# Kernel tuning notes

Hardware: AMD Instinct MI355X
Metric: run time of the kernel (lower is better)

Reference implementation:

```python
import jax, jax.numpy as jnp
import numpy as np

D_MODEL = 1024
NUM_HEADS = 16
D_K = D_MODEL // NUM_HEADS


def setup_inputs() -> dict:
    key = jax.random.key(0)
    ks = jax.random.split(key, 11)
    B, S = 2, 2048
    scale = 1.0 / np.sqrt(D_MODEL)
    inp = {
        "Q": jax.random.normal(ks[0], (B, S, D_MODEL), jnp.float32),
        "K": jax.random.normal(ks[1], (B, S, D_MODEL), jnp.float32),
        "V": jax.random.normal(ks[2], (B, S, D_MODEL), jnp.float32),
        # per-head projection weights stacked on head axis: [H, d_model, d_k]
        "Wq": jax.random.uniform(ks[3], (NUM_HEADS, D_MODEL, D_K), jnp.float32, -scale, scale),
        "bq": jax.random.uniform(ks[4], (NUM_HEADS, D_K), jnp.float32, -scale, scale),
        "Wk": jax.random.uniform(ks[5], (NUM_HEADS, D_MODEL, D_K), jnp.float32, -scale, scale),
        "bk": jax.random.uniform(ks[6], (NUM_HEADS, D_K), jnp.float32, -scale, scale),
        "Wv": jax.random.uniform(ks[7], (NUM_HEADS, D_MODEL, D_K), jnp.float32, -scale, scale),
        "bv": jax.random.uniform(ks[8], (NUM_HEADS, D_K), jnp.float32, -scale, scale),
        "Wo": jax.random.uniform(ks[9], (D_MODEL, D_MODEL), jnp.float32, -scale, scale),
        "bo": jax.random.uniform(ks[10], (D_MODEL,), jnp.float32, -scale, scale),
    }
    return inp


def reference(Q, K, V, Wq, bq, Wk, bk, Wv, bv, Wo, bo):
    # Batched equivalent of the per-head loop: project all heads at once.
    q = jnp.einsum("bsd,hdk->bhsk", Q, Wq) + bq[None, :, None, :]
    k = jnp.einsum("bsd,hdk->bhsk", K, Wk) + bk[None, :, None, :]
    v = jnp.einsum("bsd,hdk->bhsk", V, Wv) + bv[None, :, None, :]
    scores = jnp.einsum("bhqk,bhmk->bhqm", q, k) / jnp.sqrt(jnp.float32(D_K))
    weights = jax.nn.softmax(scores, axis=-1)
    attn = jnp.einsum("bhqm,bhmk->bhqk", weights, v)  # [B,H,S,d_k]
    B, H, S, Dk = attn.shape
    concat = attn.transpose(0, 2, 1, 3).reshape(B, S, H * Dk)  # head-order concat
    return concat @ Wo.T + bo
```

## Files before the change

kernel.cpp:

```cpp
#include <hip/hip_runtime.h>
#include <math.h>

#define BATCH 2
#define SLEN 2048
#define DM 1024
#define NH 16
#define DK 64
#define STILES (SLEN / 64)

typedef __attribute__((ext_vector_type(8))) __bf16 bf16x8;
typedef __attribute__((ext_vector_type(4))) float f32x4;

__device__ __forceinline__ unsigned short f2bf(float x) {
  unsigned u = __builtin_bit_cast(unsigned, x);
  unsigned r = (u + 0x7fffu + ((u >> 16) & 1u)) >> 16;
  return (unsigned short)r;
}
__device__ __forceinline__ void splitbf(float x, unsigned short& h,
                                        unsigned short& l) {
  unsigned u = __builtin_bit_cast(unsigned, x);
  h = (unsigned short)(u >> 16);
  float hf = __builtin_bit_cast(float, u & 0xffff0000u);
  l = (unsigned short)(__builtin_bit_cast(unsigned, x - hf) >> 16);
}

__device__ __forceinline__ void gld16(const unsigned short* g,
                                      unsigned short* l) {
  __builtin_amdgcn_global_load_lds(
      (const __attribute__((address_space(1))) void*)g,
      (__attribute__((address_space(3))) void*)l, 16, 0, 0);
}

__global__ __launch_bounds__(256)
void convert_w(const float* __restrict__ Wq, const float* __restrict__ Wk,
               const float* __restrict__ Wv, unsigned short* __restrict__ Wqt,
               unsigned short* __restrict__ Wkt,
               unsigned short* __restrict__ Wvt) {
  const int kb = blockIdx.x, h = blockIdx.y, z = blockIdx.z;
  const float* W = (z == 0 ? Wq : z == 1 ? Wk : Wv) +
                   ((size_t)h * DM + kb * 64) * DK;
  unsigned short* D = (z == 0 ? Wqt : z == 1 ? Wkt : Wvt);

  __shared__ float T[64][65];
  const int tid = threadIdx.x;
  {
    int r = tid >> 2, c0 = (tid & 3) * 16;
#pragma unroll
    for (int i = 0; i < 4; ++i) {
      float4 f = *(const float4*)(W + (size_t)r * DK + c0 + i * 4);
      T[r][c0 + i * 4 + 0] = f.x;
      T[r][c0 + i * 4 + 1] = f.y;
      T[r][c0 + i * 4 + 2] = f.z;
      T[r][c0 + i * 4 + 3] = f.w;
    }
  }
  __syncthreads();
  int j = tid >> 2, p = tid & 3;
  int n = h * 64 + j;
  int kloc = p * 16;
  unsigned short hi[16], lo[16];
#pragma unroll
  for (int i = 0; i < 16; ++i) splitbf(T[kloc + i][j], hi[i], lo[i]);
  int kglob = kb * 64 + kloc;
  int blk = kglob >> 5;
  int c0 = (kglob & 31) >> 3;
  int key = n & 7;
  unsigned short* rowp = D + (size_t)n * 2048 + blk * 64;
  uint4 u0, u1;
  u0.x = (unsigned)hi[0] | ((unsigned)hi[1] << 16);
  u0.y = (unsigned)hi[2] | ((unsigned)hi[3] << 16);
  u0.z = (unsigned)hi[4] | ((unsigned)hi[5] << 16);
  u0.w = (unsigned)hi[6] | ((unsigned)hi[7] << 16);
  u1.x = (unsigned)hi[8] | ((unsigned)hi[9] << 16);
  u1.y = (unsigned)hi[10] | ((unsigned)hi[11] << 16);
  u1.z = (unsigned)hi[12] | ((unsigned)hi[13] << 16);
  u1.w = (unsigned)hi[14] | ((unsigned)hi[15] << 16);
  *(uint4*)(rowp + ((c0 ^ key)) * 8) = u0;
  *(uint4*)(rowp + (((c0 + 1) ^ key)) * 8) = u1;
  u0.x = (unsigned)lo[0] | ((unsigned)lo[1] << 16);
  u0.y = (unsigned)lo[2] | ((unsigned)lo[3] << 16);
  u0.z = (unsigned)lo[4] | ((unsigned)lo[5] << 16);
  u0.w = (unsigned)lo[6] | ((unsigned)lo[7] << 16);
  u1.x = (unsigned)lo[8] | ((unsigned)lo[9] << 16);
  u1.y = (unsigned)lo[10] | ((unsigned)lo[11] << 16);
  u1.z = (unsigned)lo[12] | ((unsigned)lo[13] << 16);
  u1.w = (unsigned)lo[14] | ((unsigned)lo[15] << 16);
  *(uint4*)(rowp + (((c0 + 4) ^ key)) * 8) = u0;
  *(uint4*)(rowp + (((c0 + 5) ^ key)) * 8) = u1;
}

__global__ __launch_bounds__(256)
void convert_x(const float* __restrict__ Q, const float* __restrict__ K,
               const float* __restrict__ V, unsigned short* __restrict__ Xp) {
  const int m = blockIdx.x, z = blockIdx.y;
  const float* src = (z == 0 ? Q : z == 1 ? K : V) + (size_t)m * DM;
  unsigned short* dst =
      Xp + (size_t)z * (8u * 1024 * 1024) + (size_t)m * 2048;
  const int k0 = threadIdx.x * 4;
  float4 f = *(const float4*)(src + k0);
  ushort4 h4, l4;
  splitbf(f.x, h4.x, l4.x);
  splitbf(f.y, h4.y, l4.y);
  splitbf(f.z, h4.z, l4.z);
  splitbf(f.w, h4.w, l4.w);
  int blk = k0 >> 5, ch = (k0 & 31) >> 3, off = k0 & 7, key = m & 7;
  unsigned short* rowp = dst + blk * 64;
  *(ushort4*)(rowp + ((ch ^ key)) * 8 + off) = h4;
  *(ushort4*)(rowp + (((ch + 4) ^ key)) * 8 + off) = l4;
}

__global__ __launch_bounds__(256)
void convert_wo(const float* __restrict__ Wo, unsigned short* __restrict__ Wot) {
  const int n = blockIdx.x;
  const int t = threadIdx.x;
  const int k0 = t * 4;
  float4 f = *(const float4*)(Wo + (size_t)n * DM + k0);
  ushort4 h4, l4;
  splitbf(f.x, h4.x, l4.x);
  splitbf(f.y, h4.y, l4.y);
  splitbf(f.z, h4.z, l4.z);
  splitbf(f.w, h4.w, l4.w);
  int blk = k0 >> 5, ch = (k0 & 31) >> 3, off = k0 & 7, key = n & 7;
  unsigned short* rowp = Wot + (size_t)n * 2048 + blk * 64;
  *(ushort4*)(rowp + ((ch ^ key)) * 8 + off) = h4;
  *(ushort4*)(rowp + (((ch + 4) ^ key)) * 8 + off) = l4;
}

__global__ __launch_bounds__(256)
void proj_gemm(const unsigned short* __restrict__ Xp,
               const unsigned short* __restrict__ Wqt,
               const unsigned short* __restrict__ Wkt,
               const unsigned short* __restrict__ Wvt,
               const float* __restrict__ bq, const float* __restrict__ bk,
               const float* __restrict__ bv, unsigned short* __restrict__ q_all,
               unsigned short* __restrict__ k_all,
               unsigned short* __restrict__ vt) {
  const int ntile = blockIdx.x, mt = blockIdx.y, z = blockIdx.z;
  const unsigned short* B = (z == 0 ? Wqt : z == 1 ? Wkt : Wvt);
  const float* bias = (z == 0 ? bq : z == 1 ? bk : bv);

  __shared__ alignas(16) unsigned short As[2][128 * 64];
  __shared__ alignas(16) unsigned short Bs[2][128 * 64];

  const int tid = threadIdx.x;
  const int lane = tid & 63, w = tid >> 6;
  const int l15 = lane & 15, quad = lane >> 4;
  const int wm = (w & 1) * 64, wn = (w >> 1) * 64;
  const int kx = l15 & 7;

  const unsigned short* Ap =
      Xp + (size_t)z * (8u * 1024 * 1024) + (size_t)(mt * 128) * 2048;
  const unsigned short* Bp = B + (size_t)(ntile * 128) * 2048;

#pragma unroll
  for (int it = 0; it < 4; ++it) {
    int s = tid + it * 256;
    int r = s >> 3, seg = s & 7;
    gld16(Ap + (size_t)r * 2048 + seg * 8, &As[0][s * 8]);
    gld16(Bp + (size_t)r * 2048 + seg * 8, &Bs[0][s * 8]);
  }

  f32x4 acc[4][4];
#pragma unroll
  for (int i = 0; i < 4; ++i)
#pragma unroll
    for (int j = 0; j < 4; ++j) acc[i][j] = (f32x4){0.f, 0.f, 0.f, 0.f};

  int cur = 0;
  for (int kk = 0; kk < 32; ++kk) {
    __syncthreads();

    if (kk + 1 < 32) {
      int blk = (kk + 1) * 64;
#pragma unroll
      for (int it = 0; it < 4; ++it) {
        int s = tid + it * 256;
        int r = s >> 3, seg = s & 7;
        gld16(Ap + (size_t)r * 2048 + blk + seg * 8, &As[cur ^ 1][s * 8]);
        gld16(Bp + (size_t)r * 2048 + blk + seg * 8, &Bs[cur ^ 1][s * 8]);
      }
    }

    bf16x8 ah[4], al[4];
#pragma unroll
    for (int i = 0; i < 4; ++i) {
      const unsigned short* p = &As[cur][(wm + i * 16 + l15) * 64];
      ah[i] = *(const bf16x8*)(p + ((quad ^ kx)) * 8);
      al[i] = *(const bf16x8*)(p + (((quad + 4) ^ kx)) * 8);
    }
#pragma unroll
    for (int j = 0; j < 4; ++j) {
      const unsigned short* p = &Bs[cur][(wn + j * 16 + l15) * 64];
      bf16x8 bh = *(const bf16x8*)(p + ((quad ^ kx)) * 8);
      bf16x8 bl = *(const bf16x8*)(p + (((quad + 4) ^ kx)) * 8);
#pragma unroll
      for (int i = 0; i < 4; ++i) {
        acc[i][j] = __builtin_amdgcn_mfma_f32_16x16x32_bf16(ah[i], bh, acc[i][j], 0, 0, 0);
        acc[i][j] = __builtin_amdgcn_mfma_f32_16x16x32_bf16(al[i], bh, acc[i][j], 0, 0, 0);
        acc[i][j] = __builtin_amdgcn_mfma_f32_16x16x32_bf16(ah[i], bl, acc[i][j], 0, 0, 0);
      }
    }
    cur ^= 1;
  }

  if (z <= 1) {
    unsigned short* dst = (z == 0 ? q_all : k_all);
#pragma unroll
    for (int i = 0; i < 4; ++i)
#pragma unroll
      for (int j = 0; j < 4; ++j) {
        int n = ntile * 128 + wn + j * 16 + l15;
        int hh_ = n >> 6, d = n & 63;
        int chi = (d >> 5) * 8 + ((d & 31) >> 3);
        float bn = bias[n];
#pragma unroll
        for (int r = 0; r < 4; ++r) {
          int m = mt * 128 + wm + i * 16 + quad * 4 + r;
          int key = m & 15;
          size_t rb = (size_t)m * 2048 + hh_ * 128;
          unsigned short hv, lv;
          splitbf(acc[i][j][r] + bn, hv, lv);
          dst[rb + ((chi ^ key)) * 8 + (d & 7)] = hv;
          dst[rb + (((chi + 4) ^ key)) * 8 + (d & 7)] = lv;
        }
      }
  } else {
#pragma unroll
    for (int i = 0; i < 4; ++i)
#pragma unroll
      for (int j = 0; j < 4; ++j) {
        int n = ntile * 128 + wn + j * 16 + l15;
        int h = n >> 6, d = n & 63;
        float bn = bias[n];
        int m0 = mt * 128 + wm + i * 16 + quad * 4;
        int b = m0 >> 11, s0_ = m0 & 2047;
        int kt = s0_ >> 6, sl = s0_ & 63;
        int ch = sl >> 3, off = sl & 7, key = d & 15;
        ushort4 h4, l4;
        splitbf(acc[i][j][0] + bn, h4.x, l4.x);
        splitbf(acc[i][j][1] + bn, h4.y, l4.y);
        splitbf(acc[i][j][2] + bn, h4.z, l4.z);
        splitbf(acc[i][j][3] + bn, h4.w, l4.w);
        size_t base =
            (size_t)(b * NH + h) * 262144 + (size_t)d * 4096 + kt * 128;
        *(ushort4*)(vt + base + ((ch ^ key)) * 8 + off) = h4;
        *(ushort4*)(vt + base + (((ch + 8) ^ key)) * 8 + off) = l4;
      }
  }
}

__global__ __launch_bounds__(256)
void out_gemm(const unsigned short* __restrict__ a_all,
              const unsigned short* __restrict__ Wot,
              const float* __restrict__ bo, float* __restrict__ out) {
  const int ntile = blockIdx.x, mt = blockIdx.y;

  __shared__ alignas(16) unsigned short As[2][64 * 64];
  __shared__ alignas(16) unsigned short Bs[2][128 * 64];

  const int tid = threadIdx.x;
  const int lane = tid & 63, w = tid >> 6;
  const int l15 = lane & 15, quad = lane >> 4;
  const int wn = w * 32;
  const int kx = l15 & 7;

  const unsigned short* Ap = a_all + (size_t)(mt * 64) * 2048;
  const unsigned short* Bp = Wot + (size_t)(ntile * 128) * 2048;

#pragma unroll
  for (int it = 0; it < 2; ++it) {
    int s = tid + it * 256;
    int r = s >> 3, seg = s & 7;
    gld16(Ap + (size_t)r * 2048 + seg * 8, &As[0][s * 8]);
  }
#pragma unroll
  for (int it = 0; it < 4; ++it) {
    int s = tid + it * 256;
    int r = s >> 3, seg = s & 7;
    gld16(Bp + (size_t)r * 2048 + seg * 8, &Bs[0][s * 8]);
  }

  f32x4 acc[4][2];
#pragma unroll
  for (int i = 0; i < 4; ++i)
#pragma unroll
    for (int j = 0; j < 2; ++j) acc[i][j] = (f32x4){0.f, 0.f, 0.f, 0.f};

  int cur = 0;
  for (int kk = 0; kk < 32; ++kk) {
    __syncthreads();

    if (kk + 1 < 32) {
      int blk = (kk + 1) * 64;
#pragma unroll
      for (int it = 0; it < 2; ++it) {
        int s = tid + it * 256;
        int r = s >> 3, seg = s & 7;
        gld16(Ap + (size_t)r * 2048 + blk + seg * 8, &As[cur ^ 1][s * 8]);
      }
#pragma unroll
      for (int it = 0; it < 4; ++it) {
        int s = tid + it * 256;
        int r = s >> 3, seg = s & 7;
        gld16(Bp + (size_t)r * 2048 + blk + seg * 8, &Bs[cur ^ 1][s * 8]);
      }
    }

    bf16x8 ah[4], al[4];
#pragma unroll
    for (int i = 0; i < 4; ++i) {
      const unsigned short* p = &As[cur][(i * 16 + l15) * 64];
      ah[i] = *(const bf16x8*)(p + ((quad ^ kx)) * 8);
      al[i] = *(const bf16x8*)(p + (((quad + 4) ^ kx)) * 8);
    }
#pragma unroll
    for (int j = 0; j < 2; ++j) {
      const unsigned short* p = &Bs[cur][(wn + j * 16 + l15) * 64];
      bf16x8 bh = *(const bf16x8*)(p + ((quad ^ kx)) * 8);
      bf16x8 bl = *(const bf16x8*)(p + (((quad + 4) ^ kx)) * 8);
#pragma unroll
      for (int i = 0; i < 4; ++i) {
        acc[i][j] = __builtin_amdgcn_mfma_f32_16x16x32_bf16(ah[i], bh, acc[i][j], 0, 0, 0);
        acc[i][j] = __builtin_amdgcn_mfma_f32_16x16x32_bf16(al[i], bh, acc[i][j], 0, 0, 0);
        acc[i][j] = __builtin_amdgcn_mfma_f32_16x16x32_bf16(ah[i], bl, acc[i][j], 0, 0, 0);
      }
    }
    cur ^= 1;
  }

#pragma unroll
  for (int i = 0; i < 4; ++i)
#pragma unroll
    for (int j = 0; j < 2; ++j) {
      int n = ntile * 128 + wn + j * 16 + l15;
      float bn = bo[n];
#pragma unroll
      for (int r = 0; r < 4; ++r) {
        int m = mt * 64 + i * 16 + quad * 4 + r;
        out[(size_t)m * DM + n] = acc[i][j][r] + bn;
      }
    }
}

__global__ __launch_bounds__(256)
void attn_kernel(const unsigned short* __restrict__ q_all,
                 const unsigned short* __restrict__ k_all,
                 const unsigned short* __restrict__ vt,
                 unsigned short* __restrict__ a_all) {
  const int qt = blockIdx.x, h = blockIdx.y, b = blockIdx.z;
  const unsigned short* vp = vt + (size_t)(b * NH + h) * 262144;

  __shared__ alignas(16) unsigned short Ks[2][64 * 128];
  __shared__ alignas(16) unsigned short Vs[2][64 * 128];
  __shared__ alignas(16) unsigned short Ps[128 * 64];

  const int tid = threadIdx.x;
  const int lane = tid & 63;
  const int w = tid >> 6;
  const int l15 = lane & 15;
  const int quad = lane >> 4;

  bf16x8 qf[2][2][2];
#pragma unroll
  for (int rt = 0; rt < 2; ++rt) {
    const unsigned short* qrow =
        q_all + (size_t)(b * SLEN + qt * 128 + w * 32 + rt * 16 + l15) * 2048 +
        h * 128;
#pragma unroll
    for (int kb = 0; kb < 2; ++kb) {
      qf[rt][kb][0] = *(const bf16x8*)(qrow + ((kb * 8 + quad) ^ l15) * 8);
      qf[rt][kb][1] = *(const bf16x8*)(qrow + ((kb * 8 + quad + 4) ^ l15) * 8);
    }
  }

  {
    const unsigned short* ksrc = k_all + (size_t)(b * SLEN) * 2048 + h * 128;
#pragma unroll
    for (int it = 0; it < 4; ++it) {
      int ss = it * 256 + tid;
      int r = ss >> 4, p = ss & 15;
      gld16(ksrc + (size_t)r * 2048 + p * 8, &Ks[0][ss * 8]);
    }
#pragma unroll
    for (int it = 0; it < 4; ++it) {
      int ss = it * 256 + tid;
      int d = ss >> 4, p = ss & 15;
      gld16(vp + (size_t)d * 4096 + p * 8, &Vs[0][ss * 8]);
    }
  }

  f32x4 o[2][4];
  float lpart[2][4];
#pragma unroll
  for (int rt = 0; rt < 2; ++rt)
#pragma unroll
    for (int nt = 0; nt < 4; ++nt) {
      o[rt][nt] = (f32x4){0.f, 0.f, 0.f, 0.f};
      lpart[rt][nt] = 0.f;
    }

  int cur = 0;
  for (int kt = 0; kt < STILES; ++kt) {
    __syncthreads();

    if (kt + 1 < STILES) {
      const unsigned short* ksrc =
          k_all + (size_t)(b * SLEN + (kt + 1) * 64) * 2048 + h * 128;
#pragma unroll
      for (int it = 0; it < 4; ++it) {
        int ss = it * 256 + tid;
        int r = ss >> 4, p = ss & 15;
        gld16(ksrc + (size_t)r * 2048 + p * 8, &Ks[cur ^ 1][ss * 8]);
      }
#pragma unroll
      for (int it = 0; it < 4; ++it) {
        int ss = it * 256 + tid;
        int d = ss >> 4, p = ss & 15;
        gld16(vp + (size_t)d * 4096 + (kt + 1) * 128 + p * 8,
              &Vs[cur ^ 1][ss * 8]);
      }
    }

    f32x4 sc[2][4];
#pragma unroll
    for (int rt = 0; rt < 2; ++rt)
#pragma unroll
      for (int ct = 0; ct < 4; ++ct) sc[rt][ct] = (f32x4){0.f, 0.f, 0.f, 0.f};
#pragma unroll
    for (int ct = 0; ct < 4; ++ct) {
      const unsigned short* kbase = &Ks[cur][(ct * 16 + l15) * 128];
#pragma unroll
      for (int kb = 0; kb < 2; ++kb) {
        bf16x8 kh = *(const bf16x8*)(kbase + ((kb * 8 + quad) ^ l15) * 8);
        bf16x8 kl = *(const bf16x8*)(kbase + ((kb * 8 + quad + 4) ^ l15) * 8);
#pragma unroll
        for (int rt = 0; rt < 2; ++rt) {
          sc[rt][ct] = __builtin_amdgcn_mfma_f32_16x16x32_bf16(qf[rt][kb][0], kh, sc[rt][ct], 0, 0, 0);
          sc[rt][ct] = __builtin_amdgcn_mfma_f32_16x16x32_bf16(qf[rt][kb][0], kl, sc[rt][ct], 0, 0, 0);
          sc[rt][ct] = __builtin_amdgcn_mfma_f32_16x16x32_bf16(qf[rt][kb][1], kh, sc[rt][ct], 0, 0, 0);
        }
      }
    }

#pragma unroll
    for (int rt = 0; rt < 2; ++rt)
#pragma unroll
      for (int ct = 0; ct < 4; ++ct)
#pragma unroll
        for (int r = 0; r < 4; ++r) {
          float e = __expf(sc[rt][ct][r] * 0.125f);
          lpart[rt][r] += e;
          int prow = w * 32 + rt * 16 + quad * 4 + r;
          int pkey = (prow >> 1) & 7;
          Ps[prow * 64 + (((ct * 2 + (l15 >> 3)) ^ pkey)) * 8 + (l15 & 7)] =
              f2bf(e);
        }
    __syncthreads();

    int rk = (l15 >> 1) & 7;
#pragma unroll
    for (int kb = 0; kb < 2; ++kb) {
      bf16x8 pf[2];
#pragma unroll
      for (int rt = 0; rt < 2; ++rt)
        pf[rt] = *(const bf16x8*)(&Ps[(w * 32 + rt * 16 + l15) * 64 +
                                      (((kb * 4 + quad) ^ rk)) * 8]);
#pragma unroll
      for (int nt = 0; nt < 4; ++nt) {
        const unsigned short* vb = &Vs[cur][(nt * 16 + l15) * 128];
        bf16x8 vh = *(const bf16x8*)(vb + (((kb * 4 + quad) ^ l15)) * 8);
        bf16x8 vl = *(const bf16x8*)(vb + (((kb * 4 + quad + 8) ^ l15)) * 8);
#pragma unroll
        for (int rt = 0; rt < 2; ++rt) {
          o[rt][nt] = __builtin_amdgcn_mfma_f32_16x16x32_bf16(pf[rt], vh, o[rt][nt], 0, 0, 0);
          o[rt][nt] = __builtin_amdgcn_mfma_f32_16x16x32_bf16(pf[rt], vl, o[rt][nt], 0, 0, 0);
        }
      }
    }
    __syncthreads();
    cur ^= 1;
  }

#pragma unroll
  for (int rt = 0; rt < 2; ++rt) {
    float inv[4];
#pragma unroll
    for (int r = 0; r < 4; ++r) {
      float lv = lpart[rt][r];
#pragma unroll
      for (int m = 1; m < 16; m <<= 1) lv += __shfl_xor(lv, m, 64);
      inv[r] = 1.f / lv;
    }
#pragma unroll
    for (int nt = 0; nt < 4; ++nt) {
      int c = h * 64 + nt * 16 + l15;
      int Bb = c >> 5;
      int d32 = c & 31;
      int ch = d32 >> 3, off = d32 & 7;
#pragma unroll
      for (int r = 0; r < 4; ++r) {
        float val = o[rt][nt][r] * inv[r];
        int srow = qt * 128 + w * 32 + rt * 16 + quad * 4 + r;
        int key = srow & 7;
        size_t g = (size_t)(b * SLEN + srow) * 2048 + Bb * 64;
        unsigned short hv, lv2;
        splitbf(val, hv, lv2);
        a_all[g + ((ch ^ key)) * 8 + off] = hv;
        a_all[g + (((ch + 4) ^ key)) * 8 + off] = lv2;
      }
    }
  }
}

extern "C" void kernel_launch(void* const* d_in, const int* in_sizes, int n_in,
                              void* d_out, int out_size, void* d_ws,
                              size_t ws_size, hipStream_t stream) {
  (void)in_sizes; (void)n_in; (void)out_size; (void)ws_size;
  const float* Q = (const float*)d_in[0];
  const float* K = (const float*)d_in[1];
  const float* V = (const float*)d_in[2];
  const float* Wq = (const float*)d_in[3];
  const float* bq = (const float*)d_in[4];
  const float* Wk = (const float*)d_in[5];
  const float* bk = (const float*)d_in[6];
  const float* Wv = (const float*)d_in[7];
  const float* bv = (const float*)d_in[8];
  const float* Wo = (const float*)d_in[9];
  const float* bo = (const float*)d_in[10];
  float* out = (float*)d_out;

  unsigned short* us = (unsigned short*)d_ws;
  const size_t M8 = 8u * 1024 * 1024;
  unsigned short* q_all = us;
  unsigned short* k_all = us + M8;
  unsigned short* vt = us + 2 * M8;
  unsigned short* a_all = us + 3 * M8;
  unsigned short* Wqt = a_all;
  unsigned short* Wkt = a_all + 2 * 1024 * 1024;
  unsigned short* Wvt = a_all + 4 * 1024 * 1024;
  unsigned short* Xp = us + 4 * M8;
  unsigned short* Wot = q_all;

  convert_w<<<dim3(16, 16, 3), 256, 0, stream>>>(Wq, Wk, Wv, Wqt, Wkt, Wvt);
  convert_x<<<dim3(4096, 3), 256, 0, stream>>>(Q, K, V, Xp);
  proj_gemm<<<dim3(8, 32, 3), 256, 0, stream>>>(Xp, Wqt, Wkt, Wvt, bq, bk, bv,
                                                q_all, k_all, vt);
  attn_kernel<<<dim3(SLEN / 128, NH, BATCH), 256, 0, stream>>>(q_all, k_all,
                                                               vt, a_all);
  convert_wo<<<dim3(1024), 256, 0, stream>>>(Wo, Wot);
  out_gemm<<<dim3(8, 64), 256, 0, stream>>>(a_all, Wot, bo, out);
}
```

Before: 369.7 us.

## Restructure projection GEMM into 256x256 tiles with ping-pong phased pipeline

```diff
diff --git a/kernel.cpp b/kernel.cpp
--- a/kernel.cpp
+++ b/kernel.cpp
@@ -126,7 +126,7 @@
   *(ushort4*)(rowp + (((ch + 4) ^ key)) * 8 + off) = l4;
 }
 
-__global__ __launch_bounds__(256)
+__global__ __launch_bounds__(512, 2)
 void proj_gemm(const unsigned short* __restrict__ Xp,
                const unsigned short* __restrict__ Wqt,
                const unsigned short* __restrict__ Wkt,
@@ -136,116 +136,169 @@
                unsigned short* __restrict__ k_all,
                unsigned short* __restrict__ vt) {
   const int ntile = blockIdx.x, mt = blockIdx.y, z = blockIdx.z;
-  const unsigned short* B = (z == 0 ? Wqt : z == 1 ? Wkt : Wvt);
+  const unsigned short* Bw = (z == 0 ? Wqt : z == 1 ? Wkt : Wvt);
   const float* bias = (z == 0 ? bq : z == 1 ? bk : bv);
 
-  __shared__ alignas(16) unsigned short As[2][128 * 64];
-  __shared__ alignas(16) unsigned short Bs[2][128 * 64];
+  __shared__ alignas(16) unsigned short As[2][256 * 64];
+  __shared__ alignas(16) unsigned short Bs[2][256 * 64];
 
   const int tid = threadIdx.x;
   const int lane = tid & 63, w = tid >> 6;
   const int l15 = lane & 15, quad = lane >> 4;
-  const int wm = (w & 1) * 64, wn = (w >> 1) * 64;
+  const int wm = (w >> 2) * 128, wn = (w & 3) * 64;
   const int kx = l15 & 7;
+  const int r0 = tid >> 3, seg = tid & 7;
 
   const unsigned short* Ap =
-      Xp + (size_t)z * (8u * 1024 * 1024) + (size_t)(mt * 128) * 2048;
-  const unsigned short* Bp = B + (size_t)(ntile * 128) * 2048;
-
-#pragma unroll
-  for (int it = 0; it < 4; ++it) {
-    int s = tid + it * 256;
-    int r = s >> 3, seg = s & 7;
-    gld16(Ap + (size_t)r * 2048 + seg * 8, &As[0][s * 8]);
-    gld16(Bp + (size_t)r * 2048 + seg * 8, &Bs[0][s * 8]);
-  }
-
-  f32x4 acc[4][4];
-#pragma unroll
-  for (int i = 0; i < 4; ++i)
-#pragma unroll
-    for (int j = 0; j < 4; ++j) acc[i][j] = (f32x4){0.f, 0.f, 0.f, 0.f};
-
-  int cur = 0;
-  for (int kk = 0; kk < 32; ++kk) {
-    __syncthreads();
-
-    if (kk + 1 < 32) {
-      int blk = (kk + 1) * 64;
-#pragma unroll
-      for (int it = 0; it < 4; ++it) {
-        int s = tid + it * 256;
-        int r = s >> 3, seg = s & 7;
-        gld16(Ap + (size_t)r * 2048 + blk + seg * 8, &As[cur ^ 1][s * 8]);
-        gld16(Bp + (size_t)r * 2048 + blk + seg * 8, &Bs[cur ^ 1][s * 8]);
-      }
-    }
-
-    bf16x8 ah[4], al[4];
-#pragma unroll
-    for (int i = 0; i < 4; ++i) {
-      const unsigned short* p = &As[cur][(wm + i * 16 + l15) * 64];
-      ah[i] = *(const bf16x8*)(p + ((quad ^ kx)) * 8);
-      al[i] = *(const bf16x8*)(p + (((quad + 4) ^ kx)) * 8);
-    }
-#pragma unroll
-    for (int j = 0; j < 4; ++j) {
-      const unsigned short* p = &Bs[cur][(wn + j * 16 + l15) * 64];
-      bf16x8 bh = *(const bf16x8*)(p + ((quad ^ kx)) * 8);
-      bf16x8 bl = *(const bf16x8*)(p + (((quad + 4) ^ kx)) * 8);
-#pragma unroll
-      for (int i = 0; i < 4; ++i) {
-        acc[i][j] = __builtin_amdgcn_mfma_f32_16x16x32_bf16(ah[i], bh, acc[i][j], 0, 0, 0);
-        acc[i][j] = __builtin_amdgcn_mfma_f32_16x16x32_bf16(al[i], bh, acc[i][j], 0, 0, 0);
-        acc[i][j] = __builtin_amdgcn_mfma_f32_16x16x32_bf16(ah[i], bl, acc[i][j], 0, 0, 0);
-      }
-    }
-    cur ^= 1;
-  }
+      Xp + (size_t)z * (8u * 1024 * 1024) + (size_t)(mt * 256) * 2048;
+  const unsigned short* Bp = Bw + (size_t)(ntile * 256) * 2048;
+
+#define STAGE_A(bf, hh, t)                                                    \
+  do {                                                                        \
+    const unsigned short* _s =                                                \
+        Ap + (size_t)((hh)*64 + r0) * 2048 + (t)*64 + seg * 8;                \
+    unsigned short* _d = &As[bf][((hh)*64 + r0) * 64 + seg * 8];              \
+    gld16(_s, _d);                                                            \
+    gld16(_s + (size_t)128 * 2048, _d + 128 * 64);                            \
+  } while (0)
+#define STAGE_B(bf, hh, t)                                                    \
+  do {                                                                        \
+    int _rb = ((r0 >> 5) << 6) + (hh)*32 + (r0 & 31);                         \
+    const unsigned short* _s = Bp + (size_t)_rb * 2048 + (t)*64 + seg * 8;    \
+    unsigned short* _d = &Bs[bf][_rb * 64 + seg * 8];                         \
+    gld16(_s, _d);                                                            \
+    gld16(_s + (size_t)128 * 2048, _d + 128 * 64);                            \
+  } while (0)
+#define VMW(n) asm volatile("s_waitcnt vmcnt(" #n ")" ::: "memory")
+
+#define PHASE(BUF, QM, QN, STG, VMS)                                          \
+  do {                                                                        \
+    bf16x8 ah_[4], al_[4], bh_[2], bl_[2];                                    \
+    _Pragma("unroll") for (int i_ = 0; i_ < 4; ++i_) {                        \
+      const unsigned short* p_ =                                              \
+          &As[BUF][(wm + (QM)*64 + i_ * 16 + l15) * 64];                      \
+      ah_[i_] = *(const bf16x8*)(p_ + ((quad ^ kx)) * 8);                     \
+      al_[i_] = *(const bf16x8*)(p_ + (((quad + 4) ^ kx)) * 8);               \
+    }                                                                         \
+    _Pragma("unroll") for (int j_ = 0; j_ < 2; ++j_) {                        \
+      const unsigned short* p_ =                                              \
+          &Bs[BUF][(wn + (QN)*32 + j_ * 16 + l15) * 64];                      \
+      bh_[j_] = *(const bf16x8*)(p_ + ((quad ^ kx)) * 8);                     \
+      bl_[j_] = *(const bf16x8*)(p_ + (((quad + 4) ^ kx)) * 8);               \
+    }                                                                         \
+    STG;                                                                      \
+    VMS;                                                                      \
+    asm volatile("s_waitcnt lgkmcnt(8)" ::: "memory");                        \
+    __builtin_amdgcn_s_barrier();                                             \
+    asm volatile("s_waitcnt lgkmcnt(0)" ::: "memory");                        \
+    __builtin_amdgcn_sched_barrier(0);                                        \
+    __builtin_amdgcn_s_setprio(1);                                            \
+    _Pragma("unroll") for (int j_ = 0; j_ < 2; ++j_)                          \
+        _Pragma("unroll") for (int i_ = 0; i_ < 4; ++i_) {                    \
+      acc[QM][QN][i_][j_] = __builtin_amdgcn_mfma_f32_16x16x32_bf16(          \
+          ah_[i_], bh_[j_], acc[QM][QN][i_][j_], 0, 0, 0);                    \
+      acc[QM][QN][i_][j_] = __builtin_amdgcn_mfma_f32_16x16x32_bf16(          \
+          al_[i_], bh_[j_], acc[QM][QN][i_][j_], 0, 0, 0);                    \
+      acc[QM][QN][i_][j_] = __builtin_amdgcn_mfma_f32_16x16x32_bf16(          \
+          ah_[i_], bl_[j_], acc[QM][QN][i_][j_], 0, 0, 0);                    \
+    }                                                                         \
+    __builtin_amdgcn_s_setprio(0);                                            \
+    __builtin_amdgcn_sched_barrier(0);                                        \
+    __builtin_amdgcn_s_barrier();                                             \
+  } while (0)
+
+  f32x4 acc[2][2][4][2];
+#pragma unroll
+  for (int a0 = 0; a0 < 2; ++a0)
+#pragma unroll
+    for (int a1 = 0; a1 < 2; ++a1)
+#pragma unroll
+      for (int a2 = 0; a2 < 4; ++a2)
+#pragma unroll
+        for (int a3 = 0; a3 < 2; ++a3)
+          acc[a0][a1][a2][a3] = (f32x4){0.f, 0.f, 0.f, 0.f};
+
+  STAGE_B(0, 0, 0);
+  STAGE_A(0, 0, 0);
+  STAGE_A(0, 1, 0);
+  STAGE_B(0, 1, 0);
+  STAGE_B(1, 0, 1);
+  STAGE_A(1, 0, 1);
+  VMW(4);
+  __builtin_amdgcn_s_barrier();
+
+#pragma unroll 1
+  for (int it2 = 0; it2 < 16; ++it2) {
+    const int O = 2 * it2 + 1;
+    const int En = 2 * it2 + 2;
+    const int On = 2 * it2 + 3;
+    const bool sE = (it2 < 15);
+    PHASE(0, 0, 0, STAGE_A(1, 1, O), (void)0);
+    PHASE(0, 1, 0, STAGE_B(1, 1, O), (void)0);
+    PHASE(0, 0, 1, if (sE) STAGE_B(0, 0, En), (void)0);
+    PHASE(0, 1, 1, if (sE) STAGE_A(0, 0, En),
+          if (sE) { VMW(4); } else { VMW(0); });
+    PHASE(1, 0, 0, if (sE) STAGE_A(0, 1, En), (void)0);
+    PHASE(1, 1, 0, if (sE) STAGE_B(0, 1, En), (void)0);
+    PHASE(1, 0, 1, if (sE) STAGE_B(1, 0, On), (void)0);
+    PHASE(1, 1, 1, if (sE) STAGE_A(1, 0, On), if (sE) VMW(4));
+  }
+#undef PHASE
+#undef VMW
+#undef STAGE_A
+#undef STAGE_B
 
   if (z <= 1) {
     unsigned short* dst = (z == 0 ? q_all : k_all);
 #pragma unroll
-    for (int i = 0; i < 4; ++i)
-#pragma unroll
-      for (int j = 0; j < 4; ++j) {
-        int n = ntile * 128 + wn + j * 16 + l15;
-        int hh_ = n >> 6, d = n & 63;
-        int chi = (d >> 5) * 8 + ((d & 31) >> 3);
-        float bn = bias[n];
-#pragma unroll
-        for (int r = 0; r < 4; ++r) {
-          int m = mt * 128 + wm + i * 16 + quad * 4 + r;
-          int key = m & 15;
-          size_t rb = (size_t)m * 2048 + hh_ * 128;
-          unsigned short hv, lv;
-          splitbf(acc[i][j][r] + bn, hv, lv);
-          dst[rb + ((chi ^ key)) * 8 + (d & 7)] = hv;
-          dst[rb + (((chi + 4) ^ key)) * 8 + (d & 7)] = lv;
-        }
-      }
+    for (int qm = 0; qm < 2; ++qm)
+#pragma unroll
+      for (int qn = 0; qn < 2; ++qn)
+#pragma unroll
+        for (int i = 0; i < 4; ++i)
+#pragma unroll
+          for (int j = 0; j < 2; ++j) {
+            int n = ntile * 256 + wn + qn * 32 + j * 16 + l15;
+            int hh_ = n >> 6, d = n & 63;
+            int chi = (d >> 5) * 8 + ((d & 31) >> 3);
+            float bn = bias[n];
+#pragma unroll
+            for (int r = 0; r < 4; ++r) {
+              int m = mt * 256 + wm + qm * 64 + i * 16 + quad * 4 + r;
+              int key = m & 15;
+              size_t rb = (size_t)m * 2048 + hh_ * 128;
+              unsigned short hv, lv;
+              splitbf(acc[qm][qn][i][j][r] + bn, hv, lv);
+              dst[rb + ((chi ^ key)) * 8 + (d & 7)] = hv;
+              dst[rb + (((chi + 4) ^ key)) * 8 + (d & 7)] = lv;
+            }
+          }
   } else {
 #pragma unroll
-    for (int i = 0; i < 4; ++i)
-#pragma unroll
-      for (int j = 0; j < 4; ++j) {
-        int n = ntile * 128 + wn + j * 16 + l15;
-        int h = n >> 6, d = n & 63;
-        float bn = bias[n];
-        int m0 = mt * 128 + wm + i * 16 + quad * 4;
-        int b = m0 >> 11, s0_ = m0 & 2047;
-        int kt = s0_ >> 6, sl = s0_ & 63;
-        int ch = sl >> 3, off = sl & 7, key = d & 15;
-        ushort4 h4, l4;
-        splitbf(acc[i][j][0] + bn, h4.x, l4.x);
-        splitbf(acc[i][j][1] + bn, h4.y, l4.y);
-        splitbf(acc[i][j][2] + bn, h4.z, l4.z);
-        splitbf(acc[i][j][3] + bn, h4.w, l4.w);
-        size_t base =
-            (size_t)(b * NH + h) * 262144 + (size_t)d * 4096 + kt * 128;
-        *(ushort4*)(vt + base + ((ch ^ key)) * 8 + off) = h4;
-        *(ushort4*)(vt + base + (((ch + 8) ^ key)) * 8 + off) = l4;
-      }
+    for (int qm = 0; qm < 2; ++qm)
+#pragma unroll
+      for (int qn = 0; qn < 2; ++qn)
+#pragma unroll
+        for (int i = 0; i < 4; ++i)
+#pragma unroll
+          for (int j = 0; j < 2; ++j) {
+            int n = ntile * 256 + wn + qn * 32 + j * 16 + l15;
+            int h = n >> 6, d = n & 63;
+            float bn = bias[n];
+            int m0 = mt * 256 + wm + qm * 64 + i * 16 + quad * 4;
+            int b = m0 >> 11, s0_ = m0 & 2047;
+            int kt = s0_ >> 6, sl = s0_ & 63;
+            int ch = sl >> 3, off = sl & 7, key = d & 15;
+            ushort4 h4, l4;
+            splitbf(acc[qm][qn][i][j][0] + bn, h4.x, l4.x);
+            splitbf(acc[qm][qn][i][j][1] + bn, h4.y, l4.y);
+            splitbf(acc[qm][qn][i][j][2] + bn, h4.z, l4.z);
+            splitbf(acc[qm][qn][i][j][3] + bn, h4.w, l4.w);
+            size_t base =
+                (size_t)(b * NH + h) * 262144 + (size_t)d * 4096 + kt * 128;
+            *(ushort4*)(vt + base + ((ch ^ key)) * 8 + off) = h4;
+            *(ushort4*)(vt + base + (((ch + 8) ^ key)) * 8 + off) = l4;
+          }
   }
 }
 
@@ -543,7 +596,7 @@
 
   convert_w<<<dim3(16, 16, 3), 256, 0, stream>>>(Wq, Wk, Wv, Wqt, Wkt, Wvt);
   convert_x<<<dim3(4096, 3), 256, 0, stream>>>(Q, K, V, Xp);
-  proj_gemm<<<dim3(8, 32, 3), 256, 0, stream>>>(Xp, Wqt, Wkt, Wvt, bq, bk, bv,
+  proj_gemm<<<dim3(4, 16, 3), 512, 0, stream>>>(Xp, Wqt, Wkt, Wvt, bq, bk, bv,
                                                 q_all, k_all, vt);
   attn_kernel<<<dim3(SLEN / 128, NH, BATCH), 256, 0, stream>>>(q_all, k_all,
                                                                vt, a_all);
```

Result: faster. 361.3 us (-2.3%).
